# Kernel tuning notes

Measured on AMD Instinct MI355X. Metric: run time of the kernel, lower is better.

## Reference

```python
import jax, jax.numpy as jnp
import numpy as np

K = 16  # neighbors, matches init k


def _knn_indices(points, k):
    # points: (N, 3) -> idx: (N, k), self excluded
    sq = jnp.sum(points ** 2, axis=-1, keepdims=True)          # (N, 1)
    dist2 = sq + sq.T - 2.0 * (points @ points.T)              # (N, N)
    dist2 = jnp.clip(dist2, 0.0)
    n = points.shape[0]
    diag = jnp.eye(n, dtype=bool)
    dist2 = jnp.where(diag, jnp.inf, dist2)
    _, idx = jax.lax.top_k(-dist2, k)                          # smallest k
    return idx


def _features_single(xyz, normals, k):
    # xyz, normals: (N, 3)
    idx = _knn_indices(xyz, k)                                 # (N, k)
    neighbors = xyz[idx]                                       # (N, k, 3)
    centroid = neighbors.mean(axis=1, keepdims=True)           # (N, 1, 3)
    centered = neighbors - centroid                            # (N, k, 3)
    cov = jnp.einsum('nki,nkj->nij', centered, centered) / max(k - 1, 1)  # (N, 3, 3)
    w, v = jnp.linalg.eigh(cov.astype(jnp.float32))            # ascending
    w = w[:, ::-1].astype(xyz.dtype)                           # descending (N, 3)
    v = v[:, :, ::-1].astype(xyz.dtype)                        # (N, 3, 3)
    pca_normal = v[:, :, 2]                                    # smallest-variance dir
    dot = jnp.sum(pca_normal * normals, axis=-1, keepdims=True)
    pca_normal = pca_normal * jnp.sign(dot)
    consistency = jnp.abs(dot)                                 # (N, 1)
    total_var = jnp.clip(w.sum(axis=-1, keepdims=True), 1e-8)
    curvature = w[:, 2:3] / total_var                          # (N, 1)
    perp = jnp.abs(jnp.sum(centered * pca_normal[:, None, :], axis=-1))  # (N, k)
    roughness = perp.mean(axis=-1, keepdims=True)              # (N, 1)
    return jnp.concatenate([consistency, normals, curvature, roughness], axis=-1)


def setup_inputs() -> dict:
    key = jax.random.key(0)
    k1, k2 = jax.random.split(key)
    B, N = 2, 12288
    xyz = jax.random.normal(k1, (B, N, 3), dtype=jnp.float32)
    nrm = jax.random.normal(k2, (B, N, 3), dtype=jnp.float32)
    nrm = nrm / jnp.linalg.norm(nrm, axis=-1, keepdims=True)   # unit normals
    return {"xyz": xyz, "normals": nrm}


def reference(xyz, normals):
    return jax.vmap(lambda p, n: _features_single(p, n, K))(xyz, normals)
```

## Files before the change

### kernel.cpp

```cpp
#include <hip/hip_runtime.h>


#define NPTS 12288
#define NBATCH 2
#define NQ (NPTS * NBATCH)
#define KNN 16
#define NCH 16
#define CHSZ (NPTS / NCH)
#define MKEEP 8
#define QBLK (NQ / 256)

typedef unsigned long long u64;
typedef unsigned short u16;
typedef unsigned int u32;

#define SWAPU(a, b) { u32 _lo = min(a, b); u32 _hi = max(a, b); a = _lo; b = _hi; }
#define DIST(dst, px, py, pz) { float _dx = Qx - (px); float _dy = Qy - (py); float _dz = Qz - (pz); \
                                dst = fmaf(_dz, _dz, fmaf(_dy, _dy, _dx * _dx)); }
#define KEY(kk, dd, rel) { kk = (__float_as_uint(dd) & 0xFFFFFC00u) | (u32)(rel); }

__device__ __forceinline__ u64 shfl_xor_u64(u64 v, int mask) {
  u32 lo = (u32)v, hi = (u32)(v >> 32);
  lo = (u32)__shfl_xor((int)lo, mask);
  hi = (u32)__shfl_xor((int)hi, mask);
  return ((u64)hi << 32) | lo;
}

__global__ __launch_bounds__(256) void pack_kernel(const float* __restrict__ xyz,
                                                   float* __restrict__ xs,
                                                   float* __restrict__ ys,
                                                   float* __restrict__ zs,
                                                   float* __restrict__ ps) {
  int i = blockIdx.x * 256 + threadIdx.x;
  if (i < NQ) {
    float x = xyz[3 * i + 0], y = xyz[3 * i + 1], z = xyz[3 * i + 2];
    xs[i] = x; ys[i] = y; zs[i] = z;
    ps[i] = fmaf(z, z, fmaf(y, y, x * x));
  }
}

__global__ __launch_bounds__(256) void knn_kernel(const float* __restrict__ xs,
                                                  const float* __restrict__ ys,
                                                  const float* __restrict__ zs,
                                                  const float* __restrict__ ps,
                                                  u16* __restrict__ cidx) {
  int bid = blockIdx.x;
  int qb = bid % QBLK;
  int ch = bid / QBLK;
  int q = qb * 256 + threadIdx.x;
  int b = q / NPTS;
  int base = b * NPTS + ch * CHSZ;

  __shared__ __align__(16) float lx[CHSZ + 8];
  __shared__ __align__(16) float ly[CHSZ + 8];
  __shared__ __align__(16) float lz[CHSZ + 8];
  __shared__ __align__(16) float lp[CHSZ + 8];
  {
    float4* sx = (float4*)lx; float4* sy = (float4*)ly;
    float4* sz = (float4*)lz; float4* sp = (float4*)lp;
    const float4* gx = (const float4*)(xs + base);
    const float4* gy = (const float4*)(ys + base);
    const float4* gz = (const float4*)(zs + base);
    const float4* gp = (const float4*)(ps + base);
    if (threadIdx.x < CHSZ / 4) {
      sx[threadIdx.x] = gx[threadIdx.x];
      sy[threadIdx.x] = gy[threadIdx.x];
      sz[threadIdx.x] = gz[threadIdx.x];
      sp[threadIdx.x] = gp[threadIdx.x];
    }
  }
  __syncthreads();

  float Qx = xs[q], Qy = ys[q], Qz = zs[q];
  float qq = fmaf(Qz, Qz, fmaf(Qy, Qy, Qx * Qx));
  float m2x = -2.0f * Qx, m2y = -2.0f * Qy, m2z = -2.0f * Qz;

  u32 r0 = ~0u, r1 = ~0u, r2 = ~0u, r3 = ~0u, r4 = ~0u, r5 = ~0u, r6 = ~0u, r7 = ~0u;
  const float4* lx4 = (const float4*)lx;
  const float4* ly4 = (const float4*)ly;
  const float4* lz4 = (const float4*)lz;
  const float4* lp4 = (const float4*)lp;

#define SVAL(dst, px, py, pz, pp) dst = fmaf(m2x, (px), fmaf(m2y, (py), fmaf(m2z, (pz), qq + (pp))));

#pragma unroll 2
  for (int c0 = 0; c0 < CHSZ; c0 += 8) {
    int i4 = c0 >> 2;
    float4 xA = lx4[i4], xB = lx4[i4 + 1];
    float4 yA = ly4[i4], yB = ly4[i4 + 1];
    float4 zA = lz4[i4], zB = lz4[i4 + 1];
    float4 pA = lp4[i4], pB = lp4[i4 + 1];
    float e0, e1, e2, e3, e4, e5, e6, e7;
    SVAL(e0, xA.x, yA.x, zA.x, pA.x) SVAL(e1, xA.y, yA.y, zA.y, pA.y)
    SVAL(e2, xA.z, yA.z, zA.z, pA.z) SVAL(e3, xA.w, yA.w, zA.w, pA.w)
    SVAL(e4, xB.x, yB.x, zB.x, pB.x) SVAL(e5, xB.y, yB.y, zB.y, pB.y)
    SVAL(e6, xB.z, yB.z, zB.z, pB.z) SVAL(e7, xB.w, yB.w, zB.w, pB.w)
    u32 d0, d1, d2, d3, d4, d5, d6, d7;
    KEY(d0, e0, c0 + 0); KEY(d1, e1, c0 + 1); KEY(d2, e2, c0 + 2); KEY(d3, e3, c0 + 3);
    KEY(d4, e4, c0 + 4); KEY(d5, e5, c0 + 5); KEY(d6, e6, c0 + 6); KEY(d7, e7, c0 + 7);
    SWAPU(d0, d1) SWAPU(d2, d3) SWAPU(d4, d5) SWAPU(d6, d7)
    SWAPU(d0, d2) SWAPU(d1, d3) SWAPU(d4, d6) SWAPU(d5, d7)
    SWAPU(d1, d2) SWAPU(d5, d6)
    SWAPU(d0, d4) SWAPU(d1, d5) SWAPU(d2, d6) SWAPU(d3, d7)
    SWAPU(d2, d4) SWAPU(d3, d5)
    SWAPU(d1, d2) SWAPU(d3, d4) SWAPU(d5, d6)
    u32 m0 = min(r0, d7), m1 = min(r1, d6), m2 = min(r2, d5), m3 = min(r3, d4);
    u32 m4 = min(r4, d3), m5 = min(r5, d2), m6 = min(r6, d1), m7 = min(r7, d0);
    SWAPU(m0, m4) SWAPU(m1, m5) SWAPU(m2, m6) SWAPU(m3, m7)
    SWAPU(m0, m2) SWAPU(m1, m3) SWAPU(m4, m6) SWAPU(m5, m7)
    SWAPU(m0, m1) SWAPU(m2, m3) SWAPU(m4, m5) SWAPU(m6, m7)
    r0 = m0; r1 = m1; r2 = m2; r3 = m3; r4 = m4; r5 = m5; r6 = m6; r7 = m7;
  }

  u32 cb = (u32)(ch * CHSZ);
  uint4 w;
  w.x = (cb + (r0 & 1023u)) | ((cb + (r1 & 1023u)) << 16);
  w.y = (cb + (r2 & 1023u)) | ((cb + (r3 & 1023u)) << 16);
  w.z = (cb + (r4 & 1023u)) | ((cb + (r5 & 1023u)) << 16);
  w.w = (cb + (r6 & 1023u)) | ((cb + (r7 & 1023u)) << 16);
  *(uint4*)(cidx + (size_t)q * (NCH * MKEEP) + ch * MKEEP) = w;
}

__global__ __launch_bounds__(256) void feat_kernel(const float* __restrict__ xs,
                                                   const float* __restrict__ ys,
                                                   const float* __restrict__ zs,
                                                   const float* __restrict__ normals,
                                                   const u16* __restrict__ cidx,
                                                   float* __restrict__ out) {
  __shared__ u32 selidx[4][16];
  int wid = threadIdx.x >> 6;
  int lane = threadIdx.x & 63;
  int t = blockIdx.x * 4 + wid;
  int b = t / NPTS;
  int qi = t - b * NPTS;
  int bbase = b * NPTS;

  float Qx = xs[t], Qy = ys[t], Qz = zs[t];

  u32 pair = ((const u32*)(cidx + (size_t)t * (NCH * MKEEP)))[lane];
  int ia = (int)(pair & 0xFFFFu);
  int ib = (int)(pair >> 16);
  float dA, dB;
  DIST(dA, xs[bbase + ia], ys[bbase + ia], zs[bbase + ia]);
  DIST(dB, xs[bbase + ib], ys[bbase + ib], zs[bbase + ib]);
  u64 e0 = ((u64)__float_as_uint(dA) << 32) | (u32)ia;
  u64 e1 = ((u64)__float_as_uint(dB) << 32) | (u32)ib;

#pragma unroll
  for (int k = 2; k <= 128; k <<= 1) {
#pragma unroll
    for (int j = k >> 1; j > 0; j >>= 1) {
      if (j >= 2) {
        int h = j >> 1;
        u64 p0 = shfl_xor_u64(e0, h);
        u64 p1 = shfl_xor_u64(e1, h);
        bool wantmin = (((lane & h) == 0) == (((2 * lane) & k) == 0));
        e0 = wantmin ? (p0 < e0 ? p0 : e0) : (p0 > e0 ? p0 : e0);
        e1 = wantmin ? (p1 < e1 ? p1 : e1) : (p1 > e1 ? p1 : e1);
      } else {
        bool asc = (((2 * lane) & k) == 0);
        u64 mn = e0 < e1 ? e0 : e1;
        u64 mx = e0 < e1 ? e1 : e0;
        e0 = asc ? mn : mx;
        e1 = asc ? mx : mn;
      }
    }
  }

  u32 i0 = (u32)e0 & 0xFFFFu;
  u32 i1 = (u32)e1 & 0xFFFFu;
  bool f0 = (int)i0 != qi;
  bool f1 = (int)i1 != qi;
  u64 b0 = __ballot(f0);
  u64 b1 = __ballot(f1);
  u64 lm = lane ? (~0ull >> (64 - lane)) : 0ull;
  int pre0 = __popcll(b0 & lm) + __popcll(b1 & lm);
  int pre1 = pre0 + (f0 ? 1 : 0);
  if (f0 && pre0 < KNN) selidx[wid][pre0] = i0;
  if (f1 && pre1 < KNN) selidx[wid][pre1] = i1;
  __syncthreads();

  int nidx = selidx[wid][lane & 15];
  float px = xs[bbase + nidx];
  float py = ys[bbase + nidx];
  float pz = zs[bbase + nidx];

  float sx = px, sy = py, sz = pz;
  sx += __shfl_xor(sx, 1); sy += __shfl_xor(sy, 1); sz += __shfl_xor(sz, 1);
  sx += __shfl_xor(sx, 2); sy += __shfl_xor(sy, 2); sz += __shfl_xor(sz, 2);
  sx += __shfl_xor(sx, 4); sy += __shfl_xor(sy, 4); sz += __shfl_xor(sz, 4);
  sx += __shfl_xor(sx, 8); sy += __shfl_xor(sy, 8); sz += __shfl_xor(sz, 8);
  const float invK = 1.0f / 16.0f;
  float cx = sx * invK, cy = sy * invK, cz = sz * invK;

  float dx = px - cx, dy = py - cy, dz = pz - cz;
  float c00 = dx * dx, c01 = dx * dy, c02 = dx * dz;
  float c11 = dy * dy, c12 = dy * dz, c22 = dz * dz;
#pragma unroll
  for (int m = 1; m <= 8; m <<= 1) {
    c00 += __shfl_xor(c00, m); c01 += __shfl_xor(c01, m); c02 += __shfl_xor(c02, m);
    c11 += __shfl_xor(c11, m); c12 += __shfl_xor(c12, m); c22 += __shfl_xor(c22, m);
  }
  const float inv15 = 1.0f / 15.0f;
  c00 *= inv15; c01 *= inv15; c02 *= inv15;
  c11 *= inv15; c12 *= inv15; c22 *= inv15;

  double a00 = c00, a01 = c01, a02 = c02, a11 = c11, a12 = c12, a22 = c22;
  double tr = a00 + a11 + a22;
  double qm = tr * (1.0 / 3.0);
  double p1 = a01 * a01 + a02 * a02 + a12 * a12;
  double b00 = a00 - qm, b11 = a11 - qm, b22 = a22 - qm;
  double p2 = b00 * b00 + b11 * b11 + b22 * b22 + 2.0 * p1;
  double lmin = qm;
  if (p2 > 0.0) {
    double p = sqrt(p2 * (1.0 / 6.0));
    double ip = 1.0 / p;
    double q00 = b00 * ip, q01 = a01 * ip, q02 = a02 * ip;
    double q11 = b11 * ip, q12 = a12 * ip, q22 = b22 * ip;
    double det = q00 * (q11 * q22 - q12 * q12) - q01 * (q01 * q22 - q12 * q02) +
                 q02 * (q01 * q12 - q11 * q02);
    double r = 0.5 * det;
    r = r < -1.0 ? -1.0 : (r > 1.0 ? 1.0 : r);
    double phi = acos(r) * (1.0 / 3.0);
    lmin = qm + 2.0 * p * cos(phi + 2.0943951023931953);
  }

  double m00 = a00 - lmin, m11 = a11 - lmin, m22 = a22 - lmin;
  double v0x = a01 * a12 - a02 * m11;
  double v0y = a02 * a01 - m00 * a12;
  double v0z = m00 * m11 - a01 * a01;
  double v1x = a01 * m22 - a02 * a12;
  double v1y = a02 * a02 - m00 * m22;
  double v1z = m00 * a12 - a01 * a02;
  double v2x = m11 * m22 - a12 * a12;
  double v2y = a12 * a02 - a01 * m22;
  double v2z = a01 * a12 - m11 * a02;
  double n0 = v0x * v0x + v0y * v0y + v0z * v0z;
  double n1 = v1x * v1x + v1y * v1y + v1z * v1z;
  double n2 = v2x * v2x + v2y * v2y + v2z * v2z;
  double vx, vy, vz, nn;
  if (n0 >= n1 && n0 >= n2) { vx = v0x; vy = v0y; vz = v0z; nn = n0; }
  else if (n1 >= n2)        { vx = v1x; vy = v1y; vz = v1z; nn = n1; }
  else                      { vx = v2x; vy = v2y; vz = v2z; nn = n2; }
  if (nn < 1e-60) { vx = 0.0; vy = 0.0; vz = 1.0; nn = 1.0; }
  double inn = 1.0 / sqrt(nn);
  float vxf = (float)(vx * inn), vyf = (float)(vy * inn), vzf = (float)(vz * inn);

  float s = fabsf(dx * vxf + dy * vyf + dz * vzf);
  s += __shfl_xor(s, 1);
  s += __shfl_xor(s, 2);
  s += __shfl_xor(s, 4);
  s += __shfl_xor(s, 8);

  if (lane == 0) {
    float nrx = normals[3 * (size_t)t + 0];
    float nry = normals[3 * (size_t)t + 1];
    float nrz = normals[3 * (size_t)t + 2];
    float dot = vxf * nrx + vyf * nry + vzf * nrz;
    float cons = fabsf(dot);
    float trf = c00 + c11 + c22;
    float curv = (float)lmin / fmaxf(trf, 1e-8f);
    float* o = out + (size_t)t * 6;
    o[0] = cons;
    o[1] = nrx;
    o[2] = nry;
    o[3] = nrz;
    o[4] = curv;
    o[5] = s * invK;
  }
}

extern "C" void kernel_launch(void* const* d_in, const int* in_sizes, int n_in,
                              void* d_out, int out_size, void* d_ws, size_t ws_size,
                              hipStream_t stream) {
  const float* xyz = (const float*)d_in[0];
  const float* normals = (const float*)d_in[1];
  float* out = (float*)d_out;

  float* xs = (float*)d_ws;
  float* ys = xs + NQ;
  float* zs = ys + NQ;
  float* ps = zs + NQ;
  u16* cidx = (u16*)(ps + NQ);

  pack_kernel<<<NQ / 256, 256, 0, stream>>>(xyz, xs, ys, zs, ps);
  knn_kernel<<<QBLK * NCH, 256, 0, stream>>>(xs, ys, zs, ps, cidx);
  feat_kernel<<<NQ / 4, 256, 0, stream>>>(xs, ys, zs, normals, cidx, out);
}
```

Measured before the change: 149.2 us.

## Read KNN candidates as packed float4 from global memory instead of LDS

Candidate points are now packed by the pack kernel into an AoS float4 array (x, y, z, |p|^2), and the KNN kernel reads them straight from global memory with wave-uniform addresses. The LDS staging and __syncthreads are dropped, and a software prefetch of the next 8 candidates overlaps loads with the sorting network. This removes LDS traffic and the barrier, but relies on scalar or broadcast global loads and cache hits. The prefetch reads up to 8 float4 past the chunk end, which is why the workspace is padded.

```diff
diff --git a/kernel.cpp b/kernel.cpp
--- a/kernel.cpp
+++ b/kernel.cpp
@@ -30,71 +30,46 @@
                                                    float* __restrict__ xs,
                                                    float* __restrict__ ys,
                                                    float* __restrict__ zs,
-                                                   float* __restrict__ ps) {
+                                                   float4* __restrict__ pts4) {
   int i = blockIdx.x * 256 + threadIdx.x;
   if (i < NQ) {
     float x = xyz[3 * i + 0], y = xyz[3 * i + 1], z = xyz[3 * i + 2];
     xs[i] = x; ys[i] = y; zs[i] = z;
-    ps[i] = fmaf(z, z, fmaf(y, y, x * x));
-  }
-}
-
-__global__ __launch_bounds__(256) void knn_kernel(const float* __restrict__ xs,
-                                                  const float* __restrict__ ys,
-                                                  const float* __restrict__ zs,
-                                                  const float* __restrict__ ps,
+    pts4[i] = make_float4(x, y, z, fmaf(z, z, fmaf(y, y, x * x)));
+  }
+}
+
+__global__ __launch_bounds__(256) void knn_kernel(const float4* __restrict__ pts4,
                                                   u16* __restrict__ cidx) {
   int bid = blockIdx.x;
   int qb = bid % QBLK;
-  int ch = bid / QBLK;
-  int q = qb * 256 + threadIdx.x;
-  int b = q / NPTS;
-  int base = b * NPTS + ch * CHSZ;
-
-  __shared__ __align__(16) float lx[CHSZ + 8];
-  __shared__ __align__(16) float ly[CHSZ + 8];
-  __shared__ __align__(16) float lz[CHSZ + 8];
-  __shared__ __align__(16) float lp[CHSZ + 8];
-  {
-    float4* sx = (float4*)lx; float4* sy = (float4*)ly;
-    float4* sz = (float4*)lz; float4* sp = (float4*)lp;
-    const float4* gx = (const float4*)(xs + base);
-    const float4* gy = (const float4*)(ys + base);
-    const float4* gz = (const float4*)(zs + base);
-    const float4* gp = (const float4*)(ps + base);
-    if (threadIdx.x < CHSZ / 4) {
-      sx[threadIdx.x] = gx[threadIdx.x];
-      sy[threadIdx.x] = gy[threadIdx.x];
-      sz[threadIdx.x] = gz[threadIdx.x];
-      sp[threadIdx.x] = gp[threadIdx.x];
-    }
-  }
-  __syncthreads();
-
-  float Qx = xs[q], Qy = ys[q], Qz = zs[q];
-  float qq = fmaf(Qz, Qz, fmaf(Qy, Qy, Qx * Qx));
-  float m2x = -2.0f * Qx, m2y = -2.0f * Qy, m2z = -2.0f * Qz;
+  int chk = bid / QBLK;
+  int q0 = qb * 256;
+  int b = q0 / NPTS;
+  int base = b * NPTS + chk * CHSZ;
+  int q = q0 + threadIdx.x;
+
+  float4 Q = pts4[q];
+  float qq = Q.w;
+  float m2x = -2.0f * Q.x, m2y = -2.0f * Q.y, m2z = -2.0f * Q.z;
+
+  const float4* cp = pts4 + base;
 
   u32 r0 = ~0u, r1 = ~0u, r2 = ~0u, r3 = ~0u, r4 = ~0u, r5 = ~0u, r6 = ~0u, r7 = ~0u;
-  const float4* lx4 = (const float4*)lx;
-  const float4* ly4 = (const float4*)ly;
-  const float4* lz4 = (const float4*)lz;
-  const float4* lp4 = (const float4*)lp;
-
-#define SVAL(dst, px, py, pz, pp) dst = fmaf(m2x, (px), fmaf(m2y, (py), fmaf(m2z, (pz), qq + (pp))));
-
-#pragma unroll 2
+
+#define SVAL(dst, c) dst = fmaf(m2x, (c).x, fmaf(m2y, (c).y, fmaf(m2z, (c).z, qq + (c).w)));
+
+  float4 a0 = cp[0], a1 = cp[1], a2 = cp[2], a3 = cp[3];
+  float4 a4 = cp[4], a5 = cp[5], a6 = cp[6], a7 = cp[7];
+
+#pragma unroll 1
   for (int c0 = 0; c0 < CHSZ; c0 += 8) {
-    int i4 = c0 >> 2;
-    float4 xA = lx4[i4], xB = lx4[i4 + 1];
-    float4 yA = ly4[i4], yB = ly4[i4 + 1];
-    float4 zA = lz4[i4], zB = lz4[i4 + 1];
-    float4 pA = lp4[i4], pB = lp4[i4 + 1];
+    float4 n0 = cp[c0 + 8], n1 = cp[c0 + 9], n2 = cp[c0 + 10], n3 = cp[c0 + 11];
+    float4 n4 = cp[c0 + 12], n5 = cp[c0 + 13], n6 = cp[c0 + 14], n7 = cp[c0 + 15];
+
     float e0, e1, e2, e3, e4, e5, e6, e7;
-    SVAL(e0, xA.x, yA.x, zA.x, pA.x) SVAL(e1, xA.y, yA.y, zA.y, pA.y)
-    SVAL(e2, xA.z, yA.z, zA.z, pA.z) SVAL(e3, xA.w, yA.w, zA.w, pA.w)
-    SVAL(e4, xB.x, yB.x, zB.x, pB.x) SVAL(e5, xB.y, yB.y, zB.y, pB.y)
-    SVAL(e6, xB.z, yB.z, zB.z, pB.z) SVAL(e7, xB.w, yB.w, zB.w, pB.w)
+    SVAL(e0, a0) SVAL(e1, a1) SVAL(e2, a2) SVAL(e3, a3)
+    SVAL(e4, a4) SVAL(e5, a5) SVAL(e6, a6) SVAL(e7, a7)
     u32 d0, d1, d2, d3, d4, d5, d6, d7;
     KEY(d0, e0, c0 + 0); KEY(d1, e1, c0 + 1); KEY(d2, e2, c0 + 2); KEY(d3, e3, c0 + 3);
     KEY(d4, e4, c0 + 4); KEY(d5, e5, c0 + 5); KEY(d6, e6, c0 + 6); KEY(d7, e7, c0 + 7);
@@ -110,15 +85,18 @@
     SWAPU(m0, m2) SWAPU(m1, m3) SWAPU(m4, m6) SWAPU(m5, m7)
     SWAPU(m0, m1) SWAPU(m2, m3) SWAPU(m4, m5) SWAPU(m6, m7)
     r0 = m0; r1 = m1; r2 = m2; r3 = m3; r4 = m4; r5 = m5; r6 = m6; r7 = m7;
-  }
-
-  u32 cb = (u32)(ch * CHSZ);
+
+    a0 = n0; a1 = n1; a2 = n2; a3 = n3; a4 = n4; a5 = n5; a6 = n6; a7 = n7;
+  }
+#undef SVAL
+
+  u32 cb = (u32)(chk * CHSZ);
   uint4 w;
   w.x = (cb + (r0 & 1023u)) | ((cb + (r1 & 1023u)) << 16);
   w.y = (cb + (r2 & 1023u)) | ((cb + (r3 & 1023u)) << 16);
   w.z = (cb + (r4 & 1023u)) | ((cb + (r5 & 1023u)) << 16);
   w.w = (cb + (r6 & 1023u)) | ((cb + (r7 & 1023u)) << 16);
-  *(uint4*)(cidx + (size_t)q * (NCH * MKEEP) + ch * MKEEP) = w;
+  *(uint4*)(cidx + (size_t)q * (NCH * MKEEP) + chk * MKEEP) = w;
 }
 
 __global__ __launch_bounds__(256) void feat_kernel(const float* __restrict__ xs,
@@ -280,10 +258,10 @@
   float* xs = (float*)d_ws;
   float* ys = xs + NQ;
   float* zs = ys + NQ;
-  float* ps = zs + NQ;
-  u16* cidx = (u16*)(ps + NQ);
-
-  pack_kernel<<<NQ / 256, 256, 0, stream>>>(xyz, xs, ys, zs, ps);
-  knn_kernel<<<QBLK * NCH, 256, 0, stream>>>(xs, ys, zs, ps, cidx);
+  float4* pts4 = (float4*)(zs + NQ);
+  u16* cidx = (u16*)(pts4 + NQ + 8);
+
+  pack_kernel<<<NQ / 256, 256, 0, stream>>>(xyz, xs, ys, zs, pts4);
+  knn_kernel<<<QBLK * NCH, 256, 0, stream>>>(pts4, cidx);
   feat_kernel<<<NQ / 4, 256, 0, stream>>>(xs, ys, zs, normals, cidx, out);
 }
```

After: 155.3 us. +4.1%, slower.
